# Optimization experiments

Measured on AMD Instinct MI355X. Metric: run time of the kernel, lower is better.

Reference implementation:

```python
import jax, jax.numpy as jnp
import numpy as np

B = 8
T_SCALES = 2
SEQ_LEN = 720
PRED_LEN = 720
ENC_IN = 862
MARK = 4
D_MODEL = 256
N_HEADS = 8
D_FF = 512
D_BLOCK = 720  # == PRED_LEN -> align is Identity
E_LAYERS = 2
EPS = 1e-5


def _ln(x, g, b):
    m = x.mean(-1, keepdims=True)
    v = ((x - m) ** 2).mean(-1, keepdims=True)
    return (x - m) / jnp.sqrt(v + EPS) * g + b


def setup_inputs() -> dict:
    key = jax.random.key(0)
    ks = iter(jax.random.split(key, 64))
    def rn(shape, s=0.02):
        return jax.random.normal(next(ks), shape, jnp.float32) * s
    L, d = E_LAYERS, D_MODEL
    inp = {}
    inp["multi_batch_x"] = jax.random.normal(next(ks), (B, T_SCALES, SEQ_LEN, ENC_IN), jnp.float32)
    inp["multi_batch_x_mark"] = jax.random.normal(next(ks), (B, T_SCALES, SEQ_LEN, MARK), jnp.float32)
    inp["x_dec"] = jnp.zeros((1,), jnp.float32)
    inp["x_mark_dec"] = jnp.zeros((1,), jnp.float32)
    inp["embed_w"] = rn((d, SEQ_LEN)); inp["embed_b"] = jnp.zeros((d,), jnp.float32)
    for nm in ("Wq", "Wk", "Wv", "Wo", "W3", "W4"):
        inp[nm] = rn((L, d, d))
    for nm in ("bq", "bk", "bv", "bo", "b3", "b4"):
        inp[nm] = jnp.zeros((L, d), jnp.float32)
    inp["W1"] = rn((L, D_FF, d)); inp["b1"] = jnp.zeros((L, D_FF), jnp.float32)
    inp["W2"] = rn((L, d, D_FF)); inp["b2"] = jnp.zeros((L, d), jnp.float32)
    inp["W5"] = rn((L, D_BLOCK, 2 * d)); inp["b5"] = jnp.zeros((L, D_BLOCK), jnp.float32)
    inp["W6"] = rn((L, D_BLOCK, 2 * d)); inp["b6"] = jnp.zeros((L, D_BLOCK), jnp.float32)
    inp["ln1_g"] = jnp.ones((L, d), jnp.float32); inp["ln1_b"] = jnp.zeros((L, d), jnp.float32)
    inp["ln2_g"] = jnp.ones((L, d), jnp.float32); inp["ln2_b"] = jnp.zeros((L, d), jnp.float32)
    return inp


def reference(multi_batch_x, multi_batch_x_mark, x_dec, x_mark_dec,
              embed_w, embed_b, Wq, bq, Wk, bk, Wv, bv, Wo, bo,
              W1, b1, W2, b2, W3, b3, W4, b4, W5, b5, W6, b6,
              ln1_g, ln1_b, ln2_g, ln2_b):
    H = N_HEADS
    E = D_MODEL // H
    Bc = multi_batch_x.shape[0]
    scale = 1.0 / jnp.sqrt(jnp.asarray(E, jnp.float32))
    outs = []
    for t in range(T_SCALES):
        x = multi_batch_x[:, t].transpose(0, 2, 1)            # [B, ENC_IN, S]
        mean = x.mean(-1, keepdims=True)
        std = jnp.sqrt(((x - mean) ** 2).mean(-1, keepdims=True) + EPS)
        xn = (x - mean) / std
        xm = multi_batch_x_mark[:, t].transpose(0, 2, 1)      # [B, MARK, S]
        xin = jnp.concatenate([xn, xm], axis=1)               # [B, N, S], N = ENC_IN+MARK
        h = jnp.einsum('bns,ds->bnd', xin, embed_w) + embed_b  # [B, N, d_model]
        N = xin.shape[1]
        output = jnp.zeros((Bc, N, D_BLOCK), h.dtype)
        for l in range(E_LAYERS):
            # full attention (mask_flag=False), dropout in eval mode = identity
            q = (h @ Wq[l].T + bq[l]).reshape(Bc, N, H, E)
            k = (h @ Wk[l].T + bk[l]).reshape(Bc, N, H, E)
            v = (h @ Wv[l].T + bv[l]).reshape(Bc, N, H, E)
            scores = jnp.einsum('blhe,bshe->bhls', q, k) * scale
            A = jax.nn.softmax(scores, axis=-1)
            att = jnp.einsum('bhls,bshd->blhd', A, v).reshape(Bc, N, H * E)
            x_att = att @ Wo[l].T + bo[l]
            x_ln = _ln(h - x_att, ln1_g[l], ln1_b[l])
            # 1x1 conv FFN (conv over channel dim == linear over feature dim)
            y = jax.nn.gelu(x_ln @ W1[l].T + b1[l], approximate=False) @ W2[l].T + b2[l]
            xs = x_ln - y                                      # subtract-residual
            hh = jax.nn.sigmoid(xs @ W3[l].T + b3[l]) * (xs @ W4[l].T + b4[l])
            cat = jnp.concatenate([x_att, y], axis=-1)         # [B, N, 2*d_model]
            out = jax.nn.sigmoid(cat @ W5[l].T + b5[l]) * (cat @ W6[l].T + b6[l])
            h = _ln(hh, ln2_g[l], ln2_b[l])
            output = out - output
        # align = Identity (D_BLOCK == PRED_LEN); keep first ENC_IN channels, invert scaler
        dec = output[:, :ENC_IN, :] * std + mean               # [B, ENC_IN, PRED_LEN]
        outs.append(dec.transpose(0, 2, 1))                    # [B, PRED_LEN, ENC_IN]
    return jnp.stack(outs, axis=-1).mean(axis=-1)
```

## Files before the change

### kernel.cpp

```cpp
#include <hip/hip_runtime.h>
#include <cstdint>
#include <cstddef>

#define DEV __device__ __forceinline__
#define AS1 __attribute__((address_space(1)))
#define AS3 __attribute__((address_space(3)))

typedef unsigned short u16;
typedef unsigned char u8;
typedef long long ll;

typedef __attribute__((ext_vector_type(8))) __bf16 bf16x8;
typedef __attribute__((ext_vector_type(8))) unsigned short u16x8;
typedef __attribute__((ext_vector_type(4))) float f32x4;

static constexpr int SEQ  = 720;
static constexpr int ENC  = 862;
static constexpr int NTOK = 866;
static constexpr int DM   = 256;
static constexpr int G16  = 16;
static constexpr int MTOT = G16 * NTOK;
static constexpr int KPAD = 736;
static constexpr int SPAD = 896;
static constexpr float SC2 = 0.17677669529663689f * 1.4426950408889634f;

DEV float b2f(u16 v){ union { unsigned u; float f; } x; x.u = ((unsigned)v) << 16; return x.f; }
DEV u16 f2b(float f){ union { float f; unsigned u; } x; x.f = f;
  unsigned r = x.u + 0x7fffu + ((x.u >> 16) & 1u); return (u16)(r >> 16); }
DEV bf16x8 as_bf(u16x8 v){ return __builtin_bit_cast(bf16x8, v); }

DEV void g2l(const u16* g, u16* l){
  __builtin_amdgcn_global_load_lds((AS1 void*)g, (AS3 void*)l, 16, 0, 0);
}

DEV int xcd_work(){
  int L = blockIdx.y * gridDim.x + blockIdx.x;
  int T = gridDim.x * gridDim.y;
  int x = L & 7, k = L >> 3;
  int q = T >> 3, r = T & 7;
  int mn = x < r ? x : r;
  return x*q + mn + k;
}

struct CvtJobs {
  const float* src[10];
  u16* dst[10];
  int n[10];
  int per[10];
  ll stride[10];
};
__global__ __launch_bounds__(256) void cvt_multi(CvtJobs J)
{
  int j = blockIdx.y;
  const float* s = J.src[j];
  u16* d = J.dst[j];
  int n = J.n[j], per = J.per[j];
  ll st = J.stride[j];
  for (int i = blockIdx.x*256 + threadIdx.x; i < n; i += gridDim.x*256) {
    ll di = per ? ((ll)(i/per)*st + (i%per)) : (ll)i;
    d[di] = f2b(s[i]);
  }
}

__global__ __launch_bounds__(256) void pack_bqkv(const float* __restrict__ bq,
                                                 const float* __restrict__ bk,
                                                 const float* __restrict__ bv,
                                                 float* __restrict__ out)
{
  int idx = blockIdx.x*256 + threadIdx.x;
  if (idx >= 1536) return;
  int l = idx / 768, j = idx % 768;
  float v;
  if (j < 256)      v = bq[l*256 + j];
  else if (j < 512) v = bk[l*256 + j - 256];
  else              v = bv[l*256 + j - 512];
  out[idx] = v;
}

__global__ __launch_bounds__(256) void stats_kernel(const float* __restrict__ x,
                                                    float* __restrict__ meanp,
                                                    float* __restrict__ stdp)
{
  int g = blockIdx.x >> 2;
  int c = ((blockIdx.x & 3) << 8) + threadIdx.x;
  if (c >= ENC) return;
  const float* xp = x + (ll)g * SEQ * ENC + c;
  float s = 0.f, q = 0.f;
  for (int t = 0; t < SEQ; ++t) {
    float v = xp[(ll)t * ENC];
    s += v; q += v * v;
  }
  float mn  = s * (1.f / SEQ);
  float var = q * (1.f / SEQ) - mn * mn;
  var = var < 0.f ? 0.f : var;
  meanp[g * ENC + c] = mn;
  stdp [g * ENC + c] = sqrtf(var + 1e-5f);
}

__global__ __launch_bounds__(256) void build_xin(const float* __restrict__ x,
                                                 const float* __restrict__ xm,
                                                 const float* __restrict__ meanp,
                                                 const float* __restrict__ stdp,
                                                 u16* __restrict__ xin)
{
  int g  = blockIdx.z;
  int c0 = blockIdx.x << 5, s0 = blockIdx.y << 5;
  __shared__ float tl[32][33];
  __shared__ float mn[32], isd[32];
  int tid = threadIdx.x;
  if (tid < 32) {
    int c = c0 + tid;
    float m = 0.f, s = 1.f;
    if (c < ENC) { m = meanp[g*ENC + c]; s = stdp[g*ENC + c]; }
    mn[tid] = m; isd[tid] = 1.f / s;
  }
  __syncthreads();
  int ci = tid & 31, r = tid >> 5;
  #pragma unroll
  for (int p = 0; p < 4; ++p) {
    int sl = r + (p << 3);
    int s = s0 + sl, c = c0 + ci;
    float v = 0.f;
    if (s < SEQ && c < NTOK) {
      if (c < ENC) v = (x[((ll)g*SEQ + s)*ENC + c] - mn[ci]) * isd[ci];
      else         v = xm[((ll)g*SEQ + s)*4 + (c - ENC)];
    }
    tl[sl][ci] = v;
  }
  __syncthreads();
  int si = tid & 31;
  #pragma unroll
  for (int p = 0; p < 4; ++p) {
    int cl = r + (p << 3);
    int c = c0 + cl;
    if (c < NTOK) xin[((ll)g*NTOK + c)*KPAD + s0 + si] = f2b(tl[si][cl]);
  }
}

__global__ __launch_bounds__(256) void pack_embedw(const float* __restrict__ ew,
                                                   u16* __restrict__ wp)
{
  int row = blockIdx.x;
  for (int c = threadIdx.x; c < KPAD; c += 256)
    wp[row*KPAD + c] = (c < SEQ) ? f2b(ew[row*SEQ + c]) : (u16)0;
}

__global__ __launch_bounds__(256) void transpose_v(const u16* __restrict__ v, int ldv,
                                                   u16* __restrict__ vT)
{
  int g = blockIdx.z;
  int d0 = blockIdx.x << 5, s0 = blockIdx.y << 5;
  __shared__ u16 tl[32][33];
  int tid = threadIdx.x;
  int di = tid & 31, r = tid >> 5;
  #pragma unroll
  for (int p = 0; p < 4; ++p) {
    int sl = r + (p << 3);
    int s = s0 + sl;
    u16 val = 0;
    if (s < NTOK) val = v[((ll)g*NTOK + s)*ldv + d0 + di];
    tl[sl][di] = val;
  }
  __syncthreads();
  int si = tid & 31;
  #pragma unroll
  for (int p = 0; p < 4; ++p) {
    int dl = r + (p << 3);
    vT[((ll)g*DM + d0 + dl)*SPAD + s0 + si] = tl[si][dl];
  }
}

__global__ __launch_bounds__(256) void flash_attn(const u16* __restrict__ qb,
                                                  const u16* __restrict__ kb,
                                                  int ldqk,
                                                  const u16* __restrict__ vT,
                                                  u16* __restrict__ attb)
{
  const int w = xcd_work();
  const int gh = w / 7;
  const int g = gh >> 3, h = gh & 7;
  const int q0 = (w % 7) * 128;
  const int tid = threadIdx.x, wv = tid >> 6, lane = tid & 63;
  const int q4 = lane >> 4, c16 = lane & 15;
  constexpr int PLD = 136;

  __shared__ __attribute__((aligned(16))) u16 Qs[128*32];
  __shared__ __attribute__((aligned(16))) u16 Ks[128*32];
  __shared__ __attribute__((aligned(16))) u16 Vs[32*PLD];
  __shared__ __attribute__((aligned(16))) u16 Ps[4][32*PLD];

  {
    int r = tid >> 1, sg = (tid & 1) << 4;
    int row = q0 + r; if (row > NTOK-1) row = NTOK-1;
    const u16* src = qb + ((ll)(g*NTOK + row))*ldqk + h*32 + sg;
    *(uint4*)&Qs[r*32 + sg]     = *(const uint4*)src;
    *(uint4*)&Qs[r*32 + sg + 8] = *(const uint4*)(src + 8);
  }
  __syncthreads();

  bf16x8 qf[2];
  qf[0] = as_bf(*(const u16x8*)&Qs[(wv*32 +      c16)*32 + q4*8]);
  qf[1] = as_bf(*(const u16x8*)&Qs[(wv*32 + 16 + c16)*32 + q4*8]);

  float lsum[2][4] = {{0,0,0,0},{0,0,0,0}};
  f32x4 oacc[2][2];
  oacc[0][0] = (f32x4){0,0,0,0}; oacc[0][1] = (f32x4){0,0,0,0};
  oacc[1][0] = (f32x4){0,0,0,0}; oacc[1][1] = (f32x4){0,0,0,0};

  for (int kt = 0; kt < 7; ++kt) {
    const int k0 = kt * 128;
    if (kt) __syncthreads();
    {
      int r = tid >> 1, sg = (tid & 1) << 4;
      int row = k0 + r; if (row > NTOK-1) row = NTOK-1;
      const u16* src = kb + ((ll)(g*NTOK + row))*ldqk + h*32 + sg;
      *(uint4*)&Ks[r*32 + sg]     = *(const uint4*)src;
      *(uint4*)&Ks[r*32 + sg + 8] = *(const uint4*)(src + 8);
    }
    {
      int e = tid >> 3, sg = (tid & 7) << 4;
      const u16* src = vT + ((ll)(g*DM + h*32 + e))*SPAD + k0 + sg;
      *(uint4*)&Vs[e*PLD + sg]     = *(const uint4*)src;
      *(uint4*)&Vs[e*PLD + sg + 8] = *(const uint4*)(src + 8);
    }
    __syncthreads();

    f32x4 s[2][8];
    #pragma unroll
    for (int i = 0; i < 2; ++i)
      #pragma unroll
      for (int j = 0; j < 8; ++j) s[i][j] = (f32x4){0,0,0,0};
    #pragma unroll
    for (int j = 0; j < 8; ++j) {
      bf16x8 kf = as_bf(*(const u16x8*)&Ks[(j*16 + c16)*32 + q4*8]);
      s[0][j] = __builtin_amdgcn_mfma_f32_16x16x32_bf16(qf[0], kf, s[0][j], 0, 0, 0);
      s[1][j] = __builtin_amdgcn_mfma_f32_16x16x32_bf16(qf[1], kf, s[1][j], 0, 0, 0);
    }
    if (kt == 6) {
      #pragma unroll
      for (int j = 0; j < 8; ++j) {
        if (k0 + j*16 + c16 >= NTOK) {
          #pragma unroll
          for (int r = 0; r < 4; ++r) { s[0][j][r] = -1e30f; s[1][j][r] = -1e30f; }
        }
      }
    }

    #pragma unroll
    for (int i = 0; i < 2; ++i)
      #pragma unroll
      for (int j = 0; j < 8; ++j)
        #pragma unroll
        for (int r = 0; r < 4; ++r) {
          float p = exp2f(s[i][j][r]);
          lsum[i][r] += p;
          unsigned u = __builtin_bit_cast(unsigned, p);
          Ps[wv][(i*16 + q4*4 + r)*PLD + j*16 + c16] = (u16)(u >> 16);
        }

    #pragma unroll
    for (int kk = 0; kk < 4; ++kk) {
      bf16x8 af0 = as_bf(*(const u16x8*)&Ps[wv][(     c16)*PLD + kk*32 + q4*8]);
      bf16x8 af1 = as_bf(*(const u16x8*)&Ps[wv][(16 + c16)*PLD + kk*32 + q4*8]);
      bf16x8 b0  = as_bf(*(const u16x8*)&Vs[(     c16)*PLD + kk*32 + q4*8]);
      bf16x8 b1  = as_bf(*(const u16x8*)&Vs[(16 + c16)*PLD + kk*32 + q4*8]);
      oacc[0][0] = __builtin_amdgcn_mfma_f32_16x16x32_bf16(af0, b0, oacc[0][0], 0, 0, 0);
      oacc[0][1] = __builtin_amdgcn_mfma_f32_16x16x32_bf16(af0, b1, oacc[0][1], 0, 0, 0);
      oacc[1][0] = __builtin_amdgcn_mfma_f32_16x16x32_bf16(af1, b0, oacc[1][0], 0, 0, 0);
      oacc[1][1] = __builtin_amdgcn_mfma_f32_16x16x32_bf16(af1, b1, oacc[1][1], 0, 0, 0);
    }
  }

  float linv[2][4];
  #pragma unroll
  for (int i = 0; i < 2; ++i)
    #pragma unroll
    for (int r = 0; r < 4; ++r) {
      float t = lsum[i][r];
      t += __shfl_xor(t, 1, 64);
      t += __shfl_xor(t, 2, 64);
      t += __shfl_xor(t, 4, 64);
      t += __shfl_xor(t, 8, 64);
      linv[i][r] = 1.f / t;
    }
  #pragma unroll
  for (int i = 0; i < 2; ++i)
    #pragma unroll
    for (int jn = 0; jn < 2; ++jn)
      #pragma unroll
      for (int r = 0; r < 4; ++r) {
        int row = q0 + wv*32 + i*16 + q4*4 + r;
        if (row < NTOK)
          attb[((ll)(g*NTOK + row))*DM + h*32 + jn*16 + c16] =
            f2b(oacc[i][jn][r] * linv[i][r]);
      }
}

__global__ __launch_bounds__(256) void ln_rows(const u16* __restrict__ in1,
                                               const u16* __restrict__ in2,
                                               int ld1, int ld2,
                                               const float* __restrict__ gamma,
                                               const float* __restrict__ beta,
                                               u16* __restrict__ out, int ldo, int Mrows)
{
  int row = blockIdx.x*4 + (threadIdx.x >> 6);
  int lane = threadIdx.x & 63;
  if (row >= Mrows) return;
  float xv[4];
  ushort4 a = *(const ushort4*)(in1 + (ll)row*ld1 + lane*4);
  xv[0]=b2f(a.x); xv[1]=b2f(a.y); xv[2]=b2f(a.z); xv[3]=b2f(a.w);
  if (in2) {
    ushort4 b = *(const ushort4*)(in2 + (ll)row*ld2 + lane*4);
    xv[0]-=b2f(b.x); xv[1]-=b2f(b.y); xv[2]-=b2f(b.z); xv[3]-=b2f(b.w);
  }
  float s = xv[0]+xv[1]+xv[2]+xv[3];
  #pragma unroll
  for (int o = 32; o > 0; o >>= 1) s += __shfl_xor(s, o, 64);
  float mean = s * (1.f/256.f);
  float d0=xv[0]-mean, d1=xv[1]-mean, d2=xv[2]-mean, d3=xv[3]-mean;
  float q = d0*d0 + d1*d1 + d2*d2 + d3*d3;
  #pragma unroll
  for (int o = 32; o > 0; o >>= 1) q += __shfl_xor(q, o, 64);
  float rstd = 1.f / sqrtf(q * (1.f/256.f) + 1e-5f);
  float4 gv = *(const float4*)(gamma + lane*4);
  float4 bb = *(const float4*)(beta  + lane*4);
  ushort4 o4;
  o4.x = f2b(d0*rstd*gv.x + bb.x);
  o4.y = f2b(d1*rstd*gv.y + bb.y);
  o4.z = f2b(d2*rstd*gv.z + bb.z);
  o4.w = f2b(d3*rstd*gv.w + bb.w);
  *(ushort4*)(out + (ll)row*ldo + lane*4) = o4;
}

__global__ __launch_bounds__(256) void final_combine(const u16* __restrict__ outF,
                                                     const float* __restrict__ meanp,
                                                     const float* __restrict__ stdp,
                                                     float* __restrict__ dout)
{
  int b = blockIdx.z;
  int c0 = blockIdx.x << 5, s0 = blockIdx.y << 5;
  __shared__ float tl[32][33];
  int tid = threadIdx.x;
  int si = tid & 31, r = tid >> 5;
  #pragma unroll
  for (int p = 0; p < 4; ++p) {
    int cl = r + (p << 3);
    int c = c0 + cl, s = s0 + si;
    float accv = 0.f;
    #pragma unroll
    for (int t = 0; t < 2; ++t) {
      int g = b*2 + t;
      if (c < ENC && s < SEQ) {
        float v = b2f(outF[((ll)(g*NTOK + c))*SEQ + s]);
        accv += 0.5f * (v * stdp[g*ENC + c] + meanp[g*ENC + c]);
      }
    }
    tl[cl][si] = accv;
  }
  __syncthreads();
  int ci = tid & 31;
  #pragma unroll
  for (int p = 0; p < 4; ++p) {
    int sl = r + (p << 3);
    int s = s0 + sl, c = c0 + ci;
    if (s < SEQ && c < ENC)
      dout[((ll)b*SEQ + s)*ENC + c] = tl[ci][sl];
  }
}

__global__ __launch_bounds__(256) void gemm_nt(
    const u16* __restrict__ A, const u16* __restrict__ B,
    const float* __restrict__ bias, u16* __restrict__ C,
    const u16* __restrict__ aux1, u16* __restrict__ aux2,
    int M, int N, int K, int lda, int ldb, int ldc, int ld1, int ld2, int mode)
{
  __shared__ __attribute__((aligned(16))) u16 As[128*32];
  __shared__ __attribute__((aligned(16))) u16 Bs[128*32];

  const int tid  = threadIdx.x;
  const int wv   = tid >> 6;
  const int lane = tid & 63;
  const int q4   = lane >> 4;
  const int c16  = lane & 15;

  const int w = xcd_work();
  const int n0 = (w % gridDim.x) * 128;
  const int m0 = (w / gridDim.x) * 128;
  const int wm = (wv >> 1) * 64;
  const int wn = (wv & 1) * 64;

  const int lrow = lane >> 2;
  const int lcol = (lane & 3) << 3;
  int am0 = m0 + wv*32 + lrow;      if (am0 >= M) am0 = M-1;
  int am1 = m0 + wv*32 + 16 + lrow; if (am1 >= M) am1 = M-1;
  int bn0 = n0 + wv*32 + lrow;      if (bn0 >= N) bn0 = N-1;
  int bn1 = n0 + wv*32 + 16 + lrow; if (bn1 >= N) bn1 = N-1;
  const u16* pa0 = A + (ll)am0*lda + lcol;
  const u16* pa1 = A + (ll)am1*lda + lcol;
  const u16* pb0 = B + (ll)bn0*ldb + lcol;
  const u16* pb1 = B + (ll)bn1*ldb + lcol;
  u16* dA0 = &As[(wv*32)*32];
  u16* dA1 = &As[(wv*32 + 16)*32];
  u16* dB0 = &Bs[(wv*32)*32];
  u16* dB1 = &Bs[(wv*32 + 16)*32];

  f32x4 acc[4][4];
  #pragma unroll
  for (int i = 0; i < 4; ++i)
    #pragma unroll
    for (int j = 0; j < 4; ++j) acc[i][j] = (f32x4){0,0,0,0};

  const int nk = K >> 5;
  auto issue = [&](int kt) {
    int ko = kt*32;
    g2l(pa0 + ko, dA0); g2l(pa1 + ko, dA1);
    g2l(pb0 + ko, dB0); g2l(pb1 + ko, dB1);
  };

  issue(0);
  for (int kt = 0; kt < nk; ++kt) {
    __syncthreads();

    bf16x8 af[4], bfv[4];
    #pragma unroll
    for (int i = 0; i < 4; ++i)
      af[i] = as_bf(*(const u16x8*)&As[(wm + i*16 + c16)*32 + q4*8]);
    #pragma unroll
    for (int j = 0; j < 4; ++j)
      bfv[j] = as_bf(*(const u16x8*)&Bs[(wn + j*16 + c16)*32 + q4*8]);
    #pragma unroll
    for (int i = 0; i < 4; ++i)
      #pragma unroll
      for (int j = 0; j < 4; ++j)
        acc[i][j] = __builtin_amdgcn_mfma_f32_16x16x32_bf16(af[i], bfv[j], acc[i][j], 0, 0, 0);

    if (kt + 1 < nk) { __syncthreads(); issue(kt + 1); }
  }

  #pragma unroll
  for (int i = 0; i < 4; ++i) {
    #pragma unroll
    for (int j = 0; j < 4; ++j) {
      int n = n0 + wn + j*16 + c16;
      if (n >= N) continue;
      float bv = bias ? bias[n] : 0.f;
      int mb = m0 + wm + i*16 + q4*4;
      #pragma unroll
      for (int r = 0; r < 4; ++r) {
        int m = mb + r;
        if (m >= M) continue;
        float x = acc[i][j][r] + bv;
        ll ci = (ll)m*ldc + n;
        if (mode == 0) {
          C[ci] = f2b(x);
        } else if (mode == 1) {
          C[ci] = f2b(0.5f * x * (1.f + erff(x * 0.70710678118654752f)));
        } else if (mode == 5) {
          C[ci] = f2b(n < 256 ? x * SC2 : x);
        } else {
          C[ci] = f2b(x);
          float xl = b2f(aux1[(ll)m*ld1 + n]);
          aux2[(ll)m*ld2 + n] = f2b(xl - x);
        }
      }
    }
  }
}

__global__ __launch_bounds__(256) void gemm_nt_dual(
    const u16* __restrict__ A, const u16* __restrict__ B5, const u16* __restrict__ B6,
    const float* __restrict__ bias5, const float* __restrict__ bias6,
    u16* __restrict__ C, const u16* __restrict__ sub,
    int M, int N, int K, int lda, int ldb, int ldc, int ldsub)
{
  __shared__ __attribute__((aligned(16))) u16 As[128*32];
  __shared__ __attribute__((aligned(16))) u16 B5s[64*32];
  __shared__ __attribute__((aligned(16))) u16 B6s[64*32];

  const int tid  = threadIdx.x;
  const int wv   = tid >> 6;
  const int lane = tid & 63;
  const int q4   = lane >> 4;
  const int c16  = lane & 15;

  const int w = xcd_work();
  const int n0 = (w % gridDim.x) * 64;
  const int m0 = (w / gridDim.x) * 128;
  const int wm = (wv >> 1) * 64;
  const int wn = (wv & 1) * 32;

  const int lrow = lane >> 2;
  const int lcol = (lane & 3) << 3;
  int am0 = m0 + wv*32 + lrow;      if (am0 >= M) am0 = M-1;
  int am1 = m0 + wv*32 + 16 + lrow; if (am1 >= M) am1 = M-1;
  int bn  = n0 + wv*16 + lrow;      if (bn  >= N) bn  = N-1;
  const u16* pa0 = A  + (ll)am0*lda + lcol;
  const u16* pa1 = A  + (ll)am1*lda + lcol;
  const u16* p5  = B5 + (ll)bn*ldb + lcol;
  const u16* p6  = B6 + (ll)bn*ldb + lcol;
  u16* dA0 = &As[(wv*32)*32];
  u16* dA1 = &As[(wv*32 + 16)*32];
  u16* d5  = &B5s[(wv*16)*32];
  u16* d6  = &B6s[(wv*16)*32];

  f32x4 a5[4][2], a6[4][2];
  #pragma unroll
  for (int i = 0; i < 4; ++i)
    #pragma unroll
    for (int j = 0; j < 2; ++j) { a5[i][j] = (f32x4){0,0,0,0}; a6[i][j] = (f32x4){0,0,0,0}; }

  const int nk = K >> 5;
  auto issue = [&](int kt) {
    int ko = kt*32;
    g2l(pa0 + ko, dA0); g2l(pa1 + ko, dA1);
    g2l(p5 + ko, d5);   g2l(p6 + ko, d6);
  };

  issue(0);
  for (int kt = 0; kt < nk; ++kt) {
    __syncthreads();

    bf16x8 af[4], b5f[2], b6f[2];
    #pragma unroll
    for (int i = 0; i < 4; ++i)
      af[i] = as_bf(*(const u16x8*)&As[(wm + i*16 + c16)*32 + q4*8]);
    #pragma unroll
    for (int j = 0; j < 2; ++j) {
      b5f[j] = as_bf(*(const u16x8*)&B5s[(wn + j*16 + c16)*32 + q4*8]);
      b6f[j] = as_bf(*(const u16x8*)&B6s[(wn + j*16 + c16)*32 + q4*8]);
    }
    #pragma unroll
    for (int i = 0; i < 4; ++i)
      #pragma unroll
      for (int j = 0; j < 2; ++j) {
        a5[i][j] = __builtin_amdgcn_mfma_f32_16x16x32_bf16(af[i], b5f[j], a5[i][j], 0, 0, 0);
        a6[i][j] = __builtin_amdgcn_mfma_f32_16x16x32_bf16(af[i], b6f[j], a6[i][j], 0, 0, 0);
      }

    if (kt + 1 < nk) { __syncthreads(); issue(kt + 1); }
  }

  #pragma unroll
  for (int i = 0; i < 4; ++i) {
    #pragma unroll
    for (int j = 0; j < 2; ++j) {
      int n = n0 + wn + j*16 + c16;
      if (n >= N) continue;
      float bv5 = bias5[n], bv6 = bias6[n];
      int mb = m0 + wm + i*16 + q4*4;
      #pragma unroll
      for (int r = 0; r < 4; ++r) {
        int m = mb + r;
        if (m >= M) continue;
        float z5 = a5[i][j][r] + bv5;
        float z6 = a6[i][j][r] + bv6;
        float v = z6 / (1.f + expf(-z5));
        if (sub) v -= b2f(sub[(ll)m*ldsub + n]);
        C[(ll)m*ldc + n] = f2b(v);
      }
    }
  }
}

extern "C" void kernel_launch(void* const* d_in, const int* in_sizes, int n_in,
                              void* d_out, int out_size, void* d_ws, size_t ws_size,
                              hipStream_t stream)
{
  (void)in_sizes; (void)n_in; (void)out_size; (void)ws_size;
  const float* x    = (const float*)d_in[0];
  const float* xm   = (const float*)d_in[1];
  const float* embw = (const float*)d_in[4];
  const float* embb = (const float*)d_in[5];
  const float* Wqf  = (const float*)d_in[6];
  const float* Wkf  = (const float*)d_in[7];
  const float* Wvf  = (const float*)d_in[8];
  const float* Wof  = (const float*)d_in[9];
  const float* W3f  = (const float*)d_in[10];
  const float* W4f  = (const float*)d_in[11];
  const float* bq   = (const float*)d_in[12];
  const float* bk   = (const float*)d_in[13];
  const float* bv   = (const float*)d_in[14];
  const float* bo   = (const float*)d_in[15];
  const float* b3   = (const float*)d_in[16];
  const float* b4   = (const float*)d_in[17];
  const float* W1f  = (const float*)d_in[18];
  const float* b1   = (const float*)d_in[19];
  const float* W2f  = (const float*)d_in[20];
  const float* b2   = (const float*)d_in[21];
  const float* W5f  = (const float*)d_in[22];
  const float* b5   = (const float*)d_in[23];
  const float* W6f  = (const float*)d_in[24];
  const float* b6   = (const float*)d_in[25];
  const float* ln1g = (const float*)d_in[26];
  const float* ln1b = (const float*)d_in[27];
  const float* ln2g = (const float*)d_in[28];
  const float* ln2b = (const float*)d_in[29];

  u8* ws = (u8*)d_ws;
  size_t off = 0;
  auto alloc = [&](size_t bytes) -> void* {
    void* ptr = ws + off;
    off = (off + bytes + 255) & ~(size_t)255;
    return ptr;
  };
  float* meanp = (float*)alloc((size_t)G16*ENC*4);
  float* stdp  = (float*)alloc((size_t)G16*ENC*4);
  u16* xin   = (u16*)alloc((size_t)G16*NTOK*KPAD*2);
  u16* wp    = (u16*)alloc((size_t)DM*KPAD*2);
  const int nWsm = 2*DM*DM;
  const int nWff = 2*512*DM;
  const int nW56 = 2*SEQ*512;
  u16* Wqkv = (u16*)alloc((size_t)2*768*256*2);
  u16* Wo = (u16*)alloc((size_t)nWsm*2);
  u16* W3 = (u16*)alloc((size_t)nWsm*2);
  u16* W4 = (u16*)alloc((size_t)nWsm*2);
  u16* W1 = (u16*)alloc((size_t)nWff*2);
  u16* W2 = (u16*)alloc((size_t)nWff*2);
  u16* W5 = (u16*)alloc((size_t)nW56*2);
  u16* W6 = (u16*)alloc((size_t)nW56*2);
  float* bqkv = (float*)alloc((size_t)2*768*4);
  u16* hb    = (u16*)alloc((size_t)MTOT*DM*2);
  u16* qkvb  = (u16*)alloc((size_t)MTOT*768*2);
  u16* vT    = (u16*)alloc((size_t)G16*DM*SPAD*2);
  u16* attb  = (u16*)alloc((size_t)MTOT*DM*2);
  u16* catb  = (u16*)alloc((size_t)MTOT*512*2);
  u16* xlnb  = (u16*)alloc((size_t)MTOT*DM*2);
  u16* t1b   = (u16*)alloc((size_t)MTOT*512*2);
  u16* xsb   = (u16*)alloc((size_t)MTOT*DM*2);
  u16* hhb   = (u16*)alloc((size_t)MTOT*DM*2);
  u16* out0b = (u16*)alloc((size_t)MTOT*SEQ*2);
  u16* outFb = (u16*)alloc((size_t)MTOT*SEQ*2);

  auto gemmW = [&](const u16* A, int lda, const u16* B, int ldb, const float* bias,
                   u16* C, int ldc, int M, int N, int K, int mode,
                   const u16* a1, int ld1, u16* a2, int ld2) {
    dim3 grid((N + 127) / 128, (M + 127) / 128, 1);
    gemm_nt<<<grid, 256, 0, stream>>>(A, B, bias, C, a1, a2, M, N, K,
                                      lda, ldb, ldc, ld1, ld2, mode);
  };
  auto gemmD = [&](const u16* A, int lda, const u16* B5p, const u16* B6p, int ldb,
                   const float* bias5, const float* bias6, u16* C, int ldc,
                   const u16* sub, int ldsub, int M, int N, int K) {
    dim3 grid((N + 63) / 64, (M + 127) / 128, 1);
    gemm_nt_dual<<<grid, 256, 0, stream>>>(A, B5p, B6p, bias5, bias6, C, sub,
                                           M, N, K, lda, ldb, ldc, ldsub);
  };

  CvtJobs J{};
  int nj = 0;
  auto addjob = [&](const float* s, u16* d, int n, int per, ll stride) {
    J.src[nj] = s; J.dst[nj] = d; J.n[nj] = n; J.per[nj] = per; J.stride[nj] = stride; nj++;
  };
  addjob(Wqf, Wqkv,           nWsm, 65536, 196608);
  addjob(Wkf, Wqkv + 65536,   nWsm, 65536, 196608);
  addjob(Wvf, Wqkv + 131072,  nWsm, 65536, 196608);
  addjob(Wof, Wo, nWsm, 0, 0);
  addjob(W3f, W3, nWsm, 0, 0);
  addjob(W4f, W4, nWsm, 0, 0);
  addjob(W1f, W1, nWff, 0, 0);
  addjob(W2f, W2, nWff, 0, 0);
  addjob(W5f, W5, nW56, 0, 0);
  addjob(W6f, W6, nW56, 0, 0);
  cvt_multi<<<dim3(512, 10), 256, 0, stream>>>(J);
  pack_bqkv<<<6, 256, 0, stream>>>(bq, bk, bv, bqkv);

  stats_kernel<<<64, 256, 0, stream>>>(x, meanp, stdp);
  build_xin<<<dim3(28, 23, 16), 256, 0, stream>>>(x, xm, meanp, stdp, xin);
  pack_embedw<<<256, 256, 0, stream>>>(embw, wp);

  gemmW(xin, KPAD, wp, KPAD, embb, hb, DM, MTOT, DM, KPAD, 0, nullptr, 0, nullptr, 0);

  for (int l = 0; l < 2; ++l) {
    const ll wOff = (ll)l * DM * DM;
    gemmW(hb, DM, Wqkv + (ll)l*768*256, 256, bqkv + l*768, qkvb, 768,
          MTOT, 768, DM, 5, nullptr, 0, nullptr, 0);
    transpose_v<<<dim3(8, 28, 16), 256, 0, stream>>>(qkvb + 512, 768, vT);

    flash_attn<<<dim3(7, 128), 256, 0, stream>>>(qkvb, qkvb + 256, 768, vT, attb);

    gemmW(attb, DM, Wo + wOff, DM, bo + l*DM, catb, 512, MTOT, DM, DM, 0, nullptr, 0, nullptr, 0);
    ln_rows<<<MTOT/4, 256, 0, stream>>>(hb, catb, DM, 512, ln1g + l*DM, ln1b + l*DM, xlnb, DM, MTOT);
    gemmW(xlnb, DM, W1 + (ll)l*512*DM, DM, b1 + l*512, t1b, 512, MTOT, 512, DM, 1, nullptr, 0, nullptr, 0);
    gemmW(t1b, 512, W2 + (ll)l*DM*512, 512, b2 + l*DM, catb + 256, 512, MTOT, DM, 512, 2, xlnb, DM, xsb, DM);
    gemmD(xsb, DM, W3 + wOff, W4 + wOff, DM, b3 + l*DM, b4 + l*DM, hhb, DM,
          nullptr, 0, MTOT, DM, DM);
    ln_rows<<<MTOT/4, 256, 0, stream>>>(hhb, nullptr, DM, 0, ln2g + l*DM, ln2b + l*DM, hb, DM, MTOT);
    if (l == 0)
      gemmD(catb, 512, W5 + (ll)l*SEQ*512, W6 + (ll)l*SEQ*512, 512,
            b5 + l*SEQ, b6 + l*SEQ, out0b, SEQ, nullptr, 0, MTOT, SEQ, 512);
    else
      gemmD(catb, 512, W5 + (ll)l*SEQ*512, W6 + (ll)l*SEQ*512, 512,
            b5 + l*SEQ, b6 + l*SEQ, outFb, SEQ, out0b, SEQ, MTOT, SEQ, 512);
  }

  final_combine<<<dim3(27, 23, 8), 256, 0, stream>>>(outFb, meanp, stdp, (float*)d_out);
}
```

Measured before the change: 739.4 us.

## Fuse post-attention Wo, LN, FFN, gating and output projections into one kernel

Replaces the chain of separate GEMM and layernorm launches after attention with a single per-64-row-tile kernel that keeps intermediates (x_att, x_ln, GELU hidden, y, xs, hh) in shared memory. This removes global-memory round trips for several MTOT×256/512 intermediates and about seven launches per layer. In exchange each block uses a large LDS footprint at one block per CU (launch_bounds 256,1), uses 64-row tiles with only ~217 blocks, and stages weights without double buffering, so latency hiding and occupancy may suffer.

```diff
diff --git a/kernel.cpp b/kernel.cpp
--- a/kernel.cpp
+++ b/kernel.cpp
@@ -296,42 +296,6 @@
       }
 }
 
-__global__ __launch_bounds__(256) void ln_rows(const u16* __restrict__ in1,
-                                               const u16* __restrict__ in2,
-                                               int ld1, int ld2,
-                                               const float* __restrict__ gamma,
-                                               const float* __restrict__ beta,
-                                               u16* __restrict__ out, int ldo, int Mrows)
-{
-  int row = blockIdx.x*4 + (threadIdx.x >> 6);
-  int lane = threadIdx.x & 63;
-  if (row >= Mrows) return;
-  float xv[4];
-  ushort4 a = *(const ushort4*)(in1 + (ll)row*ld1 + lane*4);
-  xv[0]=b2f(a.x); xv[1]=b2f(a.y); xv[2]=b2f(a.z); xv[3]=b2f(a.w);
-  if (in2) {
-    ushort4 b = *(const ushort4*)(in2 + (ll)row*ld2 + lane*4);
-    xv[0]-=b2f(b.x); xv[1]-=b2f(b.y); xv[2]-=b2f(b.z); xv[3]-=b2f(b.w);
-  }
-  float s = xv[0]+xv[1]+xv[2]+xv[3];
-  #pragma unroll
-  for (int o = 32; o > 0; o >>= 1) s += __shfl_xor(s, o, 64);
-  float mean = s * (1.f/256.f);
-  float d0=xv[0]-mean, d1=xv[1]-mean, d2=xv[2]-mean, d3=xv[3]-mean;
-  float q = d0*d0 + d1*d1 + d2*d2 + d3*d3;
-  #pragma unroll
-  for (int o = 32; o > 0; o >>= 1) q += __shfl_xor(q, o, 64);
-  float rstd = 1.f / sqrtf(q * (1.f/256.f) + 1e-5f);
-  float4 gv = *(const float4*)(gamma + lane*4);
-  float4 bb = *(const float4*)(beta  + lane*4);
-  ushort4 o4;
-  o4.x = f2b(d0*rstd*gv.x + bb.x);
-  o4.y = f2b(d1*rstd*gv.y + bb.y);
-  o4.z = f2b(d2*rstd*gv.z + bb.z);
-  o4.w = f2b(d3*rstd*gv.w + bb.w);
-  *(ushort4*)(out + (ll)row*ldo + lane*4) = o4;
-}
-
 __global__ __launch_bounds__(256) void final_combine(const u16* __restrict__ outF,
                                                      const float* __restrict__ meanp,
                                                      const float* __restrict__ stdp,
@@ -371,8 +335,7 @@
 __global__ __launch_bounds__(256) void gemm_nt(
     const u16* __restrict__ A, const u16* __restrict__ B,
     const float* __restrict__ bias, u16* __restrict__ C,
-    const u16* __restrict__ aux1, u16* __restrict__ aux2,
-    int M, int N, int K, int lda, int ldb, int ldc, int ld1, int ld2, int mode)
+    int M, int N, int K, int lda, int ldb, int ldc, int mode)
 {
   __shared__ __attribute__((aligned(16))) u16 As[128*32];
   __shared__ __attribute__((aligned(16))) u16 Bs[128*32];
@@ -451,114 +414,320 @@
         if (m >= M) continue;
         float x = acc[i][j][r] + bv;
         ll ci = (ll)m*ldc + n;
-        if (mode == 0) {
-          C[ci] = f2b(x);
-        } else if (mode == 1) {
-          C[ci] = f2b(0.5f * x * (1.f + erff(x * 0.70710678118654752f)));
-        } else if (mode == 5) {
-          C[ci] = f2b(n < 256 ? x * SC2 : x);
-        } else {
-          C[ci] = f2b(x);
-          float xl = b2f(aux1[(ll)m*ld1 + n]);
-          aux2[(ll)m*ld2 + n] = f2b(xl - x);
+        C[ci] = f2b(mode == 5 && n < 256 ? x * SC2 : x);
+      }
+    }
+  }
+}
+
+__global__ __launch_bounds__(256, 1) void ffn_fused(
+    const u16* __restrict__ attb, u16* __restrict__ hb,
+    const u16* __restrict__ Wo, const u16* __restrict__ W1,
+    const u16* __restrict__ W2, const u16* __restrict__ W3,
+    const u16* __restrict__ W4, const u16* __restrict__ W5,
+    const u16* __restrict__ W6,
+    const float* __restrict__ bo, const float* __restrict__ b1,
+    const float* __restrict__ b2, const float* __restrict__ b3,
+    const float* __restrict__ b4, const float* __restrict__ b5,
+    const float* __restrict__ b6,
+    const float* __restrict__ ln1g, const float* __restrict__ ln1b,
+    const float* __restrict__ ln2g, const float* __restrict__ ln2b,
+    const u16* __restrict__ sub, u16* __restrict__ outX)
+{
+  constexpr int XLD = 520;
+  constexpr int BLD = 264;
+  __shared__ __attribute__((aligned(16))) u16 bufX[64*XLD];
+  __shared__ __attribute__((aligned(16))) u16 bufB[64*BLD];
+  __shared__ __attribute__((aligned(16))) u16 bufW [256*32];
+  __shared__ __attribute__((aligned(16))) u16 bufW2[256*32];
+
+  const int tid = threadIdx.x, wv = tid >> 6, lane = tid & 63;
+  const int q4 = lane >> 4, c16 = lane & 15;
+  const int m0 = blockIdx.x * 64;
+
+  {
+    int r = tid >> 2;
+    int row = m0 + r; if (row >= MTOT) row = MTOT - 1;
+    const u16* pa = attb + (ll)row*256;
+    const u16* ph = hb   + (ll)row*256;
+    int cb = (tid & 3) * 64;
+    #pragma unroll
+    for (int p = 0; p < 8; ++p) {
+      *(uint4*)&bufX[r*XLD + cb + p*8] = *(const uint4*)(pa + cb + p*8);
+      *(uint4*)&bufB[r*BLD + cb + p*8] = *(const uint4*)(ph + cb + p*8);
+    }
+  }
+  __syncthreads();
+
+  auto stageW = [&](u16* dst, const u16* W, int ldw, int kofs, int nbase, int nmax){
+    #pragma unroll
+    for (int s = 0; s < 4; ++s) {
+      int rbase = wv*64 + s*16;
+      int row = nbase + rbase + (lane >> 2);
+      if (row > nmax) row = nmax;
+      g2l(W + (ll)row*ldw + kofs + (lane & 3)*8, dst + rbase*32);
+    }
+  };
+  auto ldA = [&](const u16* buf, int ld, int co, int i, int kt){
+    return as_bf(*(const u16x8*)&buf[(i*16 + c16)*ld + co + kt*32 + q4*8]);
+  };
+  auto ldB = [&](const u16* buf, int j){
+    return as_bf(*(const u16x8*)&buf[(wv*64 + j*16 + c16)*32 + q4*8]);
+  };
+
+  f32x4 acc[4][4];
+  #pragma unroll
+  for (int i = 0; i < 4; ++i)
+    #pragma unroll
+    for (int j = 0; j < 4; ++j) acc[i][j] = (f32x4){0,0,0,0};
+  for (int kt = 0; kt < 8; ++kt) {
+    stageW(bufW, Wo, 256, kt*32, 0, 255);
+    __syncthreads();
+    bf16x8 af[4], bb[4];
+    #pragma unroll
+    for (int i = 0; i < 4; ++i) af[i] = ldA(bufX, XLD, 0, i, kt);
+    #pragma unroll
+    for (int j = 0; j < 4; ++j) bb[j] = ldB(bufW, j);
+    #pragma unroll
+    for (int i = 0; i < 4; ++i)
+      #pragma unroll
+      for (int j = 0; j < 4; ++j)
+        acc[i][j] = __builtin_amdgcn_mfma_f32_16x16x32_bf16(af[i], bb[j], acc[i][j], 0, 0, 0);
+    __syncthreads();
+  }
+  #pragma unroll
+  for (int i = 0; i < 4; ++i)
+    #pragma unroll
+    for (int j = 0; j < 4; ++j) {
+      int n = wv*64 + j*16 + c16;
+      float bv = bo[n];
+      #pragma unroll
+      for (int r = 0; r < 4; ++r) {
+        int m = i*16 + q4*4 + r;
+        bufX[m*XLD + n] = f2b(acc[i][j][r] + bv);
+      }
+    }
+  __syncthreads();
+
+  {
+    int r = tid >> 2, cb = (tid & 3) * 64;
+    float sm = 0.f, sq = 0.f;
+    #pragma unroll
+    for (int c = 0; c < 64; c += 8) {
+      u16x8 hv = *(const u16x8*)&bufB[r*BLD + cb + c];
+      u16x8 av = *(const u16x8*)&bufX[r*XLD + cb + c];
+      #pragma unroll
+      for (int e = 0; e < 8; ++e) {
+        float d = b2f(hv[e]) - b2f(av[e]);
+        sm += d; sq += d*d;
+      }
+    }
+    sm += __shfl_xor(sm, 1, 64); sm += __shfl_xor(sm, 2, 64);
+    sq += __shfl_xor(sq, 1, 64); sq += __shfl_xor(sq, 2, 64);
+    float mu = sm * (1.f/256.f);
+    float var = sq * (1.f/256.f) - mu*mu; var = var < 0.f ? 0.f : var;
+    float rstd = 1.f / sqrtf(var + 1e-5f);
+    #pragma unroll
+    for (int c = 0; c < 64; c += 8) {
+      u16x8 hv = *(const u16x8*)&bufB[r*BLD + cb + c];
+      u16x8 av = *(const u16x8*)&bufX[r*XLD + cb + c];
+      u16x8 o;
+      #pragma unroll
+      for (int e = 0; e < 8; ++e) {
+        float d = b2f(hv[e]) - b2f(av[e]);
+        o[e] = f2b((d - mu)*rstd*ln1g[cb+c+e] + ln1b[cb+c+e]);
+      }
+      *(u16x8*)&bufB[r*BLD + cb + c] = o;
+    }
+  }
+  __syncthreads();
+
+  f32x4 yac[4][4];
+  #pragma unroll
+  for (int i = 0; i < 4; ++i)
+    #pragma unroll
+    for (int j = 0; j < 4; ++j) yac[i][j] = (f32x4){0,0,0,0};
+  #pragma unroll 1
+  for (int hf = 0; hf < 2; ++hf) {
+    f32x4 a2[4][4];
+    #pragma unroll
+    for (int i = 0; i < 4; ++i)
+      #pragma unroll
+      for (int j = 0; j < 4; ++j) a2[i][j] = (f32x4){0,0,0,0};
+    for (int kt = 0; kt < 8; ++kt) {
+      stageW(bufW, W1, 256, kt*32, hf*256, 511);
+      __syncthreads();
+      bf16x8 af[4], bb[4];
+      #pragma unroll
+      for (int i = 0; i < 4; ++i) af[i] = ldA(bufB, BLD, 0, i, kt);
+      #pragma unroll
+      for (int j = 0; j < 4; ++j) bb[j] = ldB(bufW, j);
+      #pragma unroll
+      for (int i = 0; i < 4; ++i)
+        #pragma unroll
+        for (int j = 0; j < 4; ++j)
+          a2[i][j] = __builtin_amdgcn_mfma_f32_16x16x32_bf16(af[i], bb[j], a2[i][j], 0, 0, 0);
+      __syncthreads();
+    }
+    #pragma unroll
+    for (int i = 0; i < 4; ++i)
+      #pragma unroll
+      for (int j = 0; j < 4; ++j) {
+        int n = wv*64 + j*16 + c16;
+        float bv = b1[hf*256 + n];
+        #pragma unroll
+        for (int r = 0; r < 4; ++r) {
+          int m = i*16 + q4*4 + r;
+          float xg = a2[i][j][r] + bv;
+          bufX[m*XLD + 256 + n] = f2b(0.5f*xg*(1.f + erff(xg*0.70710678118654752f)));
         }
       }
-    }
-  }
-}
-
-__global__ __launch_bounds__(256) void gemm_nt_dual(
-    const u16* __restrict__ A, const u16* __restrict__ B5, const u16* __restrict__ B6,
-    const float* __restrict__ bias5, const float* __restrict__ bias6,
-    u16* __restrict__ C, const u16* __restrict__ sub,
-    int M, int N, int K, int lda, int ldb, int ldc, int ldsub)
-{
-  __shared__ __attribute__((aligned(16))) u16 As[128*32];
-  __shared__ __attribute__((aligned(16))) u16 B5s[64*32];
-  __shared__ __attribute__((aligned(16))) u16 B6s[64*32];
-
-  const int tid  = threadIdx.x;
-  const int wv   = tid >> 6;
-  const int lane = tid & 63;
-  const int q4   = lane >> 4;
-  const int c16  = lane & 15;
-
-  const int w = xcd_work();
-  const int n0 = (w % gridDim.x) * 64;
-  const int m0 = (w / gridDim.x) * 128;
-  const int wm = (wv >> 1) * 64;
-  const int wn = (wv & 1) * 32;
-
-  const int lrow = lane >> 2;
-  const int lcol = (lane & 3) << 3;
-  int am0 = m0 + wv*32 + lrow;      if (am0 >= M) am0 = M-1;
-  int am1 = m0 + wv*32 + 16 + lrow; if (am1 >= M) am1 = M-1;
-  int bn  = n0 + wv*16 + lrow;      if (bn  >= N) bn  = N-1;
-  const u16* pa0 = A  + (ll)am0*lda + lcol;
-  const u16* pa1 = A  + (ll)am1*lda + lcol;
-  const u16* p5  = B5 + (ll)bn*ldb + lcol;
-  const u16* p6  = B6 + (ll)bn*ldb + lcol;
-  u16* dA0 = &As[(wv*32)*32];
-  u16* dA1 = &As[(wv*32 + 16)*32];
-  u16* d5  = &B5s[(wv*16)*32];
-  u16* d6  = &B6s[(wv*16)*32];
-
-  f32x4 a5[4][2], a6[4][2];
+    __syncthreads();
+    for (int kt = 0; kt < 8; ++kt) {
+      stageW(bufW, W2, 512, hf*256 + kt*32, 0, 255);
+      __syncthreads();
+      bf16x8 af[4], bb[4];
+      #pragma unroll
+      for (int i = 0; i < 4; ++i) af[i] = ldA(bufX, XLD, 256, i, kt);
+      #pragma unroll
+      for (int j = 0; j < 4; ++j) bb[j] = ldB(bufW, j);
+      #pragma unroll
+      for (int i = 0; i < 4; ++i)
+        #pragma unroll
+        for (int j = 0; j < 4; ++j)
+          yac[i][j] = __builtin_amdgcn_mfma_f32_16x16x32_bf16(af[i], bb[j], yac[i][j], 0, 0, 0);
+      __syncthreads();
+    }
+  }
   #pragma unroll
   for (int i = 0; i < 4; ++i)
     #pragma unroll
-    for (int j = 0; j < 2; ++j) { a5[i][j] = (f32x4){0,0,0,0}; a6[i][j] = (f32x4){0,0,0,0}; }
-
-  const int nk = K >> 5;
-  auto issue = [&](int kt) {
-    int ko = kt*32;
-    g2l(pa0 + ko, dA0); g2l(pa1 + ko, dA1);
-    g2l(p5 + ko, d5);   g2l(p6 + ko, d6);
-  };
-
-  issue(0);
-  for (int kt = 0; kt < nk; ++kt) {
+    for (int j = 0; j < 4; ++j) {
+      int n = wv*64 + j*16 + c16;
+      float bv = b2[n];
+      #pragma unroll
+      for (int r = 0; r < 4; ++r) {
+        int m = i*16 + q4*4 + r;
+        float y = yac[i][j][r] + bv;
+        float xl = b2f(bufB[m*BLD + n]);
+        bufX[m*XLD + 256 + n] = f2b(y);
+        bufB[m*BLD + n] = f2b(xl - y);
+      }
+    }
+  __syncthreads();
+
+  f32x4 a3[4][4], a4[4][4];
+  #pragma unroll
+  for (int i = 0; i < 4; ++i)
+    #pragma unroll
+    for (int j = 0; j < 4; ++j) { a3[i][j] = (f32x4){0,0,0,0}; a4[i][j] = (f32x4){0,0,0,0}; }
+  for (int kt = 0; kt < 8; ++kt) {
+    stageW(bufW,  W3, 256, kt*32, 0, 255);
+    stageW(bufW2, W4, 256, kt*32, 0, 255);
     __syncthreads();
-
-    bf16x8 af[4], b5f[2], b6f[2];
+    bf16x8 af[4], b3f[4], b4f[4];
+    #pragma unroll
+    for (int i = 0; i < 4; ++i) af[i] = ldA(bufB, BLD, 0, i, kt);
+    #pragma unroll
+    for (int j = 0; j < 4; ++j) { b3f[j] = ldB(bufW, j); b4f[j] = ldB(bufW2, j); }
     #pragma unroll
     for (int i = 0; i < 4; ++i)
-      af[i] = as_bf(*(const u16x8*)&As[(wm + i*16 + c16)*32 + q4*8]);
-    #pragma unroll
-    for (int j = 0; j < 2; ++j) {
-      b5f[j] = as_bf(*(const u16x8*)&B5s[(wn + j*16 + c16)*32 + q4*8]);
-      b6f[j] = as_bf(*(const u16x8*)&B6s[(wn + j*16 + c16)*32 + q4*8]);
-    }
+      #pragma unroll
+      for (int j = 0; j < 4; ++j) {
+        a3[i][j] = __builtin_amdgcn_mfma_f32_16x16x32_bf16(af[i], b3f[j], a3[i][j], 0, 0, 0);
+        a4[i][j] = __builtin_amdgcn_mfma_f32_16x16x32_bf16(af[i], b4f[j], a4[i][j], 0, 0, 0);
+      }
+    __syncthreads();
+  }
+  #pragma unroll
+  for (int i = 0; i < 4; ++i)
+    #pragma unroll
+    for (int j = 0; j < 4; ++j) {
+      int n = wv*64 + j*16 + c16;
+      float bv3 = b3[n], bv4 = b4[n];
+      #pragma unroll
+      for (int r = 0; r < 4; ++r) {
+        int m = i*16 + q4*4 + r;
+        float z3 = a3[i][j][r] + bv3;
+        float z4 = a4[i][j][r] + bv4;
+        bufB[m*BLD + n] = f2b(z4 / (1.f + expf(-z3)));
+      }
+    }
+  __syncthreads();
+
+  {
+    int r = tid >> 2, cb = (tid & 3) * 64;
+    int row = m0 + r;
+    float sm = 0.f, sq = 0.f;
+    #pragma unroll
+    for (int c = 0; c < 64; c += 8) {
+      u16x8 hv = *(const u16x8*)&bufB[r*BLD + cb + c];
+      #pragma unroll
+      for (int e = 0; e < 8; ++e) { float v = b2f(hv[e]); sm += v; sq += v*v; }
+    }
+    sm += __shfl_xor(sm, 1, 64); sm += __shfl_xor(sm, 2, 64);
+    sq += __shfl_xor(sq, 1, 64); sq += __shfl_xor(sq, 2, 64);
+    float mu = sm * (1.f/256.f);
+    float var = sq * (1.f/256.f) - mu*mu; var = var < 0.f ? 0.f : var;
+    float rstd = 1.f / sqrtf(var + 1e-5f);
+    if (row < MTOT) {
+      #pragma unroll
+      for (int c = 0; c < 64; c += 8) {
+        u16x8 hv = *(const u16x8*)&bufB[r*BLD + cb + c];
+        u16x8 o;
+        #pragma unroll
+        for (int e = 0; e < 8; ++e)
+          o[e] = f2b((b2f(hv[e]) - mu)*rstd*ln2g[cb+c+e] + ln2b[cb+c+e]);
+        *(uint4*)(hb + (ll)row*256 + cb + c) = __builtin_bit_cast(uint4, o);
+      }
+    }
+  }
+
+  #pragma unroll 1
+  for (int nc = 0; nc < 3; ++nc) {
+    int nb = nc * 256;
+    f32x4 a5[4][4], a6[4][4];
     #pragma unroll
     for (int i = 0; i < 4; ++i)
       #pragma unroll
-      for (int j = 0; j < 2; ++j) {
-        a5[i][j] = __builtin_amdgcn_mfma_f32_16x16x32_bf16(af[i], b5f[j], a5[i][j], 0, 0, 0);
-        a6[i][j] = __builtin_amdgcn_mfma_f32_16x16x32_bf16(af[i], b6f[j], a6[i][j], 0, 0, 0);
-      }
-
-    if (kt + 1 < nk) { __syncthreads(); issue(kt + 1); }
-  }
-
-  #pragma unroll
-  for (int i = 0; i < 4; ++i) {
-    #pragma unroll
-    for (int j = 0; j < 2; ++j) {
-      int n = n0 + wn + j*16 + c16;
-      if (n >= N) continue;
-      float bv5 = bias5[n], bv6 = bias6[n];
-      int mb = m0 + wm + i*16 + q4*4;
-      #pragma unroll
-      for (int r = 0; r < 4; ++r) {
-        int m = mb + r;
-        if (m >= M) continue;
-        float z5 = a5[i][j][r] + bv5;
-        float z6 = a6[i][j][r] + bv6;
-        float v = z6 / (1.f + expf(-z5));
-        if (sub) v -= b2f(sub[(ll)m*ldsub + n]);
-        C[(ll)m*ldc + n] = f2b(v);
-      }
-    }
+      for (int j = 0; j < 4; ++j) { a5[i][j] = (f32x4){0,0,0,0}; a6[i][j] = (f32x4){0,0,0,0}; }
+    for (int kt = 0; kt < 16; ++kt) {
+      stageW(bufW,  W5, 512, kt*32, nb, 719);
+      stageW(bufW2, W6, 512, kt*32, nb, 719);
+      __syncthreads();
+      bf16x8 af[4], b5f[4], b6f[4];
+      #pragma unroll
+      for (int i = 0; i < 4; ++i) af[i] = ldA(bufX, XLD, 0, i, kt);
+      #pragma unroll
+      for (int j = 0; j < 4; ++j) { b5f[j] = ldB(bufW, j); b6f[j] = ldB(bufW2, j); }
+      #pragma unroll
+      for (int i = 0; i < 4; ++i)
+        #pragma unroll
+        for (int j = 0; j < 4; ++j) {
+          a5[i][j] = __builtin_amdgcn_mfma_f32_16x16x32_bf16(af[i], b5f[j], a5[i][j], 0, 0, 0);
+          a6[i][j] = __builtin_amdgcn_mfma_f32_16x16x32_bf16(af[i], b6f[j], a6[i][j], 0, 0, 0);
+        }
+      __syncthreads();
+    }
+    #pragma unroll
+    for (int i = 0; i < 4; ++i)
+      #pragma unroll
+      for (int j = 0; j < 4; ++j) {
+        int n = nb + wv*64 + j*16 + c16;
+        if (n >= SEQ) continue;
+        float bv5 = b5[n], bv6 = b6[n];
+        #pragma unroll
+        for (int r = 0; r < 4; ++r) {
+          int m = i*16 + q4*4 + r;
+          int row = m0 + m;
+          if (row >= MTOT) continue;
+          float z5 = a5[i][j][r] + bv5;
+          float z6 = a6[i][j][r] + bv6;
+          float v = z6 / (1.f + expf(-z5));
+          if (sub) v -= b2f(sub[(ll)row*SEQ + n]);
+          outX[(ll)row*SEQ + n] = f2b(v);
+        }
+      }
   }
 }
 
@@ -623,27 +792,13 @@
   u16* qkvb  = (u16*)alloc((size_t)MTOT*768*2);
   u16* vT    = (u16*)alloc((size_t)G16*DM*SPAD*2);
   u16* attb  = (u16*)alloc((size_t)MTOT*DM*2);
-  u16* catb  = (u16*)alloc((size_t)MTOT*512*2);
-  u16* xlnb  = (u16*)alloc((size_t)MTOT*DM*2);
-  u16* t1b   = (u16*)alloc((size_t)MTOT*512*2);
-  u16* xsb   = (u16*)alloc((size_t)MTOT*DM*2);
-  u16* hhb   = (u16*)alloc((size_t)MTOT*DM*2);
   u16* out0b = (u16*)alloc((size_t)MTOT*SEQ*2);
   u16* outFb = (u16*)alloc((size_t)MTOT*SEQ*2);
 
   auto gemmW = [&](const u16* A, int lda, const u16* B, int ldb, const float* bias,
-                   u16* C, int ldc, int M, int N, int K, int mode,
-                   const u16* a1, int ld1, u16* a2, int ld2) {
+                   u16* C, int ldc, int M, int N, int K, int mode) {
     dim3 grid((N + 127) / 128, (M + 127) / 128, 1);
-    gemm_nt<<<grid, 256, 0, stream>>>(A, B, bias, C, a1, a2, M, N, K,
-                                      lda, ldb, ldc, ld1, ld2, mode);
-  };
-  auto gemmD = [&](const u16* A, int lda, const u16* B5p, const u16* B6p, int ldb,
-                   const float* bias5, const float* bias6, u16* C, int ldc,
-                   const u16* sub, int ldsub, int M, int N, int K) {
-    dim3 grid((N + 63) / 64, (M + 127) / 128, 1);
-    gemm_nt_dual<<<grid, 256, 0, stream>>>(A, B5p, B6p, bias5, bias6, C, sub,
-                                           M, N, K, lda, ldb, ldc, ldsub);
+    gemm_nt<<<grid, 256, 0, stream>>>(A, B, bias, C, M, N, K, lda, ldb, ldc, mode);
   };
 
   CvtJobs J{};
@@ -668,29 +823,27 @@
   build_xin<<<dim3(28, 23, 16), 256, 0, stream>>>(x, xm, meanp, stdp, xin);
   pack_embedw<<<256, 256, 0, stream>>>(embw, wp);
 
-  gemmW(xin, KPAD, wp, KPAD, embb, hb, DM, MTOT, DM, KPAD, 0, nullptr, 0, nullptr, 0);
-
+  gemmW(xin, KPAD, wp, KPAD, embb, hb, DM, MTOT, DM, KPAD, 0);
+
+  const int NBLK = (MTOT + 63) / 64;
   for (int l = 0; l < 2; ++l) {
-    const ll wOff = (ll)l * DM * DM;
+    const ll wOff  = (ll)l * DM * DM;
+    const ll wOff1 = (ll)l * 512 * DM;
+    const ll wOff5 = (ll)l * SEQ * 512;
     gemmW(hb, DM, Wqkv + (ll)l*768*256, 256, bqkv + l*768, qkvb, 768,
-          MTOT, 768, DM, 5, nullptr, 0, nullptr, 0);
+          MTOT, 768, DM, 5);
     transpose_v<<<dim3(8, 28, 16), 256, 0, stream>>>(qkvb + 512, 768, vT);
-
     flash_attn<<<dim3(7, 128), 256, 0, stream>>>(qkvb, qkvb + 256, 768, vT, attb);
 
-    gemmW(attb, DM, Wo + wOff, DM, bo + l*DM, catb, 512, MTOT, DM, DM, 0, nullptr, 0, nullptr, 0);
-    ln_rows<<<MTOT/4, 256, 0, stream>>>(hb, catb, DM, 512, ln1g + l*DM, ln1b + l*DM, xlnb, DM, MTOT);
-    gemmW(xlnb, DM, W1 + (ll)l*512*DM, DM, b1 + l*512, t1b, 512, MTOT, 512, DM, 1, nullptr, 0, nullptr, 0);
-    gemmW(t1b, 512, W2 + (ll)l*DM*512, 512, b2 + l*DM, catb + 256, 512, MTOT, DM, 512, 2, xlnb, DM, xsb, DM);
-    gemmD(xsb, DM, W3 + wOff, W4 + wOff, DM, b3 + l*DM, b4 + l*DM, hhb, DM,
-          nullptr, 0, MTOT, DM, DM);
-    ln_rows<<<MTOT/4, 256, 0, stream>>>(hhb, nullptr, DM, 0, ln2g + l*DM, ln2b + l*DM, hb, DM, MTOT);
-    if (l == 0)
-      gemmD(catb, 512, W5 + (ll)l*SEQ*512, W6 + (ll)l*SEQ*512, 512,
-            b5 + l*SEQ, b6 + l*SEQ, out0b, SEQ, nullptr, 0, MTOT, SEQ, 512);
-    else
-      gemmD(catb, 512, W5 + (ll)l*SEQ*512, W6 + (ll)l*SEQ*512, 512,
-            b5 + l*SEQ, b6 + l*SEQ, outFb, SEQ, out0b, SEQ, MTOT, SEQ, 512);
+    ffn_fused<<<NBLK, 256, 0, stream>>>(
+        attb, hb,
+        Wo + wOff, W1 + wOff1, W2 + wOff1, W3 + wOff, W4 + wOff,
+        W5 + wOff5, W6 + wOff5,
+        bo + l*DM, b1 + l*512, b2 + l*DM, b3 + l*DM, b4 + l*DM,
+        b5 + l*SEQ, b6 + l*SEQ,
+        ln1g + l*DM, ln1b + l*DM, ln2g + l*DM, ln2b + l*DM,
+        (l == 0) ? nullptr : out0b,
+        (l == 0) ? out0b : outFb);
   }
 
   final_combine<<<dim3(27, 23, 8), 256, 0, stream>>>(outFb, meanp, stdp, (float*)d_out);
```

New measurement: 996.3 us. 34.7% more time.
